# Optimization experiments

Measured on AMD Instinct MI355X. Metric: run time of the kernel, lower is better.

## Reference

```python
import jax, jax.numpy as jnp
import numpy as np

B, S, D, H, E, K = 4, 1024, 1024, 4096, 8, 2


def setup_inputs() -> dict:
    key = jax.random.key(0)
    ks = jax.random.split(key, 10)
    s = 0.02
    return {
        "x": jax.random.normal(ks[0], (B, S, D), jnp.float32),
        "noise": jax.random.normal(ks[1], (B, S, E), jnp.float32),
        "Wg": jax.random.normal(ks[2], (D, E), jnp.float32) * s,
        "bg": jnp.zeros((E,), jnp.float32),
        "Wn": jax.random.normal(ks[3], (D, E), jnp.float32) * s,
        "bn": jnp.zeros((E,), jnp.float32),
        "W1": jax.random.normal(ks[4], (E, D, H), jnp.float32) * s,
        "b1": jnp.zeros((E, H), jnp.float32),
        "W2": jax.random.normal(ks[5], (E, H, D), jnp.float32) * s,
        "b2": jnp.zeros((E, D), jnp.float32),
    }


def reference(x, noise, Wg, bg, Wn, bn, W1, b1, W2, b2):
    # --- noisy top-k gating ---
    logits = x @ Wg + bg                                   # [B,S,E]
    noisy = logits + noise * jax.nn.softplus(x @ Wn + bn)  # [B,S,E]
    topk_vals, topk_idx = jax.lax.top_k(noisy, K)          # [B,S,K]
    weights = jax.nn.softmax(topk_vals, axis=-1)           # [B,S,K]
    oh = jax.nn.one_hot(topk_idx, E, dtype=x.dtype)        # [B,S,K,E]
    mask = oh.sum(axis=-2)                                 # [B,S,E] 0/1 (topk idx distinct)
    w_full = (weights[..., None] * oh).sum(axis=-2)        # [B,S,E] combine weights

    # --- per-expert FFN (dense over experts, selected via w_full) ---
    h = jax.nn.gelu(jnp.einsum('bsd,edh->bseh', x, W1) + b1, approximate=False)
    eout = jnp.einsum('bseh,ehd->bsed', h, W2) + b2        # [B,S,E,D]
    combined = jnp.einsum('bse,bsed->bsd', w_full, eout)   # [B,S,D]

    # --- load balancing loss on clean gate probs ---
    gate_probs = jax.nn.softmax(logits, axis=-1)           # [B,S,E]
    expert_count = mask.sum(axis=(0, 1))                   # [E]
    total_tokens = mask.sum()
    expert_util = expert_count / total_tokens
    load_loss = jnp.sum(expert_util * gate_probs.mean(axis=(0, 1))) * E
    return combined, load_loss
```

## Files before the change

kernel.cpp:

```cpp
#include <hip/hip_runtime.h>
#include <hip/hip_bf16.h>

#define T_TOK 4096
#define D_DIM 1024
#define H_DIM 4096
#define E_EXP 8
#define K_TOP 2
#define TP (T_TOK * K_TOP)
#define BM 128
#define BN 128
#define BKS 32
#define MAX_TILES 72

typedef __attribute__((ext_vector_type(8))) short bf16x8;
typedef __attribute__((ext_vector_type(4))) float f32x4;
typedef __attribute__((ext_vector_type(8))) unsigned short u16x8;
typedef __attribute__((ext_vector_type(4))) unsigned short u16x4;

#define SWZ(row, chunk) ((chunk) ^ (((row) >> 1) & 3))

static __device__ __forceinline__ void gload16(const unsigned short* g, unsigned short* l) {
  __builtin_amdgcn_global_load_lds((const __attribute__((address_space(1))) void*)g,
                                   (__attribute__((address_space(3))) void*)l, 16, 0, 0);
}

static __device__ __forceinline__ unsigned short f2bf(float f) {
  unsigned int bits = __float_as_uint(f);
  unsigned int lsb = (bits >> 16) & 1u;
  bits += 0x7fffu + lsb;
  return (unsigned short)(bits >> 16);
}

static __device__ __forceinline__ float gelu_fast(float u) {
  float z = u * (0.79788456080286536f + 0.0356774081f * u * u);
  float t = __expf(-2.f * z);
  return u / (1.f + t);
}

#define NGATE (T_TOK / 4)
#define NTR1  ((H_DIM / 64) * (D_DIM / 64) * E_EXP)
#define NTR2  ((D_DIM / 64) * (H_DIM / 64) * E_EXP)

__global__ __launch_bounds__(256) void front_kernel(
    const float* __restrict__ W1, unsigned short* __restrict__ w1t,
    const float* __restrict__ W2, unsigned short* __restrict__ w2t,
    const float* __restrict__ x, const float* __restrict__ noise,
    const float* __restrict__ Wg, const float* __restrict__ bg,
    const float* __restrict__ Wn, const float* __restrict__ bn,
    int* __restrict__ tok_e, float* __restrict__ tok_w,
    float* __restrict__ gp_tok, int* __restrict__ counts,
    unsigned short* __restrict__ xb) {
  __shared__ float tile[64][65];
  int bid = blockIdx.x;
  const int tid = threadIdx.x;

  if (bid < NGATE) {
    const int lane = tid & 63, wid = tid >> 6;
    const int t = bid * 4 + wid;
    const float* xrow = x + (size_t)t * D_DIM;
    float ag[8] = {0, 0, 0, 0, 0, 0, 0, 0};
    float an[8] = {0, 0, 0, 0, 0, 0, 0, 0};
#pragma unroll 4
    for (int i = 0; i < 16; ++i) {
      int dd = i * 64 + lane;
      float xv = xrow[dd];
      xb[(size_t)t * D_DIM + dd] = f2bf(xv);
      const float4* g4 = (const float4*)(Wg + (size_t)dd * 8);
      const float4* n4 = (const float4*)(Wn + (size_t)dd * 8);
      float4 ga = g4[0], gb = g4[1], na = n4[0], nb = n4[1];
      ag[0] += xv * ga.x; ag[1] += xv * ga.y; ag[2] += xv * ga.z; ag[3] += xv * ga.w;
      ag[4] += xv * gb.x; ag[5] += xv * gb.y; ag[6] += xv * gb.z; ag[7] += xv * gb.w;
      an[0] += xv * na.x; an[1] += xv * na.y; an[2] += xv * na.z; an[3] += xv * na.w;
      an[4] += xv * nb.x; an[5] += xv * nb.y; an[6] += xv * nb.z; an[7] += xv * nb.w;
    }
#pragma unroll
    for (int e = 0; e < 8; ++e) {
      for (int off = 32; off > 0; off >>= 1) {
        ag[e] += __shfl_down(ag[e], off);
        an[e] += __shfl_down(an[e], off);
      }
    }
    if (lane == 0) {
      float logit[8], noisy[8];
#pragma unroll
      for (int e = 0; e < 8; ++e) {
        logit[e] = ag[e] + bg[e];
        float pre = an[e] + bn[e];
        float sp = fmaxf(pre, 0.f) + log1pf(expf(-fabsf(pre)));
        noisy[e] = logit[e] + noise[(size_t)t * 8 + e] * sp;
      }
      float mx = logit[0];
#pragma unroll
      for (int e = 1; e < 8; ++e) mx = fmaxf(mx, logit[e]);
      float s = 0.f, p[8];
#pragma unroll
      for (int e = 0; e < 8; ++e) { p[e] = expf(logit[e] - mx); s += p[e]; }
      float inv = 1.f / s;
#pragma unroll
      for (int e = 0; e < 8; ++e) gp_tok[(size_t)t * 8 + e] = p[e] * inv;
      int i0 = 0; float v0 = noisy[0];
#pragma unroll
      for (int e = 1; e < 8; ++e) if (noisy[e] > v0) { v0 = noisy[e]; i0 = e; }
      int i1 = -1; float v1 = 0.f;
#pragma unroll
      for (int e = 0; e < 8; ++e) {
        if (e == i0) continue;
        if (i1 < 0 || noisy[e] > v1) { v1 = noisy[e]; i1 = e; }
      }
      float e1 = expf(v1 - v0);
      float w0 = 1.f / (1.f + e1);
      float w1 = e1 * w0;
      tok_e[t * 2 + 0] = i0; tok_e[t * 2 + 1] = i1;
      tok_w[t * 2 + 0] = w0; tok_w[t * 2 + 1] = w1;
      atomicAdd(&counts[i0], 1);
      atomicAdd(&counts[i1], 1);
    }
    return;
  }
  bid -= NGATE;

  const float* src; unsigned short* dst; int R, C, bx, by, e;
  if (bid < NTR1) {
    R = D_DIM; C = H_DIM;
    bx = bid & 63; by = (bid >> 6) & 15; e = bid >> 10;
    src = W1; dst = w1t;
  } else {
    bid -= NTR1;
    R = H_DIM; C = D_DIM;
    bx = bid & 15; by = (bid >> 4) & 63; e = bid >> 10;
    src = W2; dst = w2t;
  }
  const int c0 = bx * 64, r0 = by * 64;
  const float* s = src + (size_t)e * R * C;
  unsigned short* d = dst + (size_t)e * R * C;

  const int rr = tid >> 4, c4 = tid & 15;
#pragma unroll
  for (int p = 0; p < 4; ++p) {
    int r = rr + p * 16;
    float4 v = *(const float4*)(&s[(size_t)(r0 + r) * C + c0 + c4 * 4]);
    tile[r][c4 * 4 + 0] = v.x;
    tile[r][c4 * 4 + 1] = v.y;
    tile[r][c4 * 4 + 2] = v.z;
    tile[r][c4 * 4 + 3] = v.w;
  }
  __syncthreads();
  const int cc = tid >> 3, r8 = tid & 7;
#pragma unroll
  for (int p = 0; p < 2; ++p) {
    int c = cc + p * 32;
    u16x8 o;
#pragma unroll
    for (int q = 0; q < 8; ++q) o[q] = f2bf(tile[r8 * 8 + q][c]);
    *(u16x8*)(&d[(size_t)(c0 + c) * R + r0 + r8 * 8]) = o;
  }
}

__global__ __launch_bounds__(256) void finalize_kernel(
    const int* __restrict__ counts, int4* __restrict__ tiles,
    int* __restrict__ ntiles,
    const int* __restrict__ tok_e, const float* __restrict__ tok_w,
    int* __restrict__ pair_token, float* __restrict__ pair_w,
    const float* __restrict__ gp_tok, float* __restrict__ out) {
  __shared__ int s_off[E_EXP];
  __shared__ int s_cur[E_EXP];
  __shared__ float red[256];
  const int tid = threadIdx.x;

  if (tid == 0) {
    int off = 0, nt = 0;
    for (int e = 0; e < E_EXP; ++e) {
      s_off[e] = off;
      int c = counts[e];
      for (int r = 0; r < c; r += BM) {
        tiles[nt] = make_int4(e, off + r, min(BM, c - r), 0);
        ++nt;
      }
      off += c;
    }
    *ntiles = nt;
  }
  if (tid < E_EXP) s_cur[tid] = 0;
  __syncthreads();

  for (int t = tid; t < T_TOK; t += 256) {
#pragma unroll
    for (int k = 0; k < 2; ++k) {
      int e = tok_e[t * 2 + k];
      int pos = atomicAdd(&s_cur[e], 1);
      int p = s_off[e] + pos;
      pair_token[p] = t;
      pair_w[p] = tok_w[t * 2 + k];
    }
  }

  float part[8] = {0, 0, 0, 0, 0, 0, 0, 0};
  for (int r = tid; r < T_TOK; r += 256) {
    const float* g = gp_tok + (size_t)r * 8;
#pragma unroll
    for (int e = 0; e < 8; ++e) part[e] += g[e];
  }
  float total[8];
#pragma unroll
  for (int e = 0; e < 8; ++e) {
    red[tid] = part[e];
    __syncthreads();
    for (int s = 128; s > 0; s >>= 1) {
      if (tid < s) red[tid] += red[tid + s];
      __syncthreads();
    }
    if (tid == 0) total[e] = red[0];
    __syncthreads();
  }
  if (tid == 0) {
    float ll = 0.f;
#pragma unroll
    for (int e = 0; e < 8; ++e)
      ll += ((float)counts[e] / (float)TP) * (total[e] / (float)T_TOK);
    out[(size_t)T_TOK * D_DIM] = ll * (float)E_EXP;
  }
}

__global__ __launch_bounds__(256) void ffn1_kernel(
    const unsigned short* __restrict__ xb,
    const unsigned short* __restrict__ w1t,
    const float* __restrict__ b1,
    const int* __restrict__ pair_token,
    const int4* __restrict__ tiles, const int* __restrict__ ntiles,
    unsigned short* __restrict__ hbuf) {
  const int NB = H_DIM / BN;
  const int nwg = MAX_TILES * NB;
  int bid = blockIdx.x;
  int wg = (bid & 7) * (nwg >> 3) + (bid >> 3);
  int tileId = wg / NB, nb = wg - tileId * NB;
  if (tileId >= *ntiles) return;
  int4 tl = tiles[tileId];
  const int e = tl.x, row0 = tl.y, rows = tl.z;
  const int n0 = nb * BN;

  __shared__ unsigned short sh[16384];
#define AS1(buf) (sh + (buf) * 4096)
#define BS1(buf) (sh + 8192 + (buf) * 4096)

  const int tid = threadIdx.x;
  const int wid = tid >> 6, lane = tid & 63;
  const int sr = tid >> 2;
  const int sc = tid & 3;
  const int scz = SWZ(sr, sc) * 8;

  int r0a = row0 + sr;       if (r0a > TP - 1) r0a = TP - 1;
  int r1a = row0 + sr + 64;  if (r1a > TP - 1) r1a = TP - 1;
  const unsigned short* a0 = xb + (size_t)pair_token[r0a] * D_DIM + scz;
  const unsigned short* a1 = xb + (size_t)pair_token[r1a] * D_DIM + scz;
  const unsigned short* bp0 = w1t + ((size_t)e * H_DIM + (n0 + sr)) * D_DIM + scz;
  const unsigned short* bp1 = w1t + ((size_t)e * H_DIM + (n0 + sr + 64)) * D_DIM + scz;

  const int wbase = wid * 512;
  const int wr = wid >> 1, wc = wid & 1;
  const int lrow = lane & 15, lkc = lane >> 4;

  f32x4 acc[4][4] = {};

  auto stage = [&](int buf, int k0) {
    gload16(a0 + k0, AS1(buf) + wbase);
    gload16(a1 + k0, AS1(buf) + wbase + 2048);
    gload16(bp0 + k0, BS1(buf) + wbase);
    gload16(bp1 + k0, BS1(buf) + wbase + 2048);
  };
  auto compute_step = [&](int buf) {
    bf16x8 af[4], bfr[4];
#pragma unroll
    for (int m = 0; m < 4; ++m) {
      int r = wr * 64 + m * 16 + lrow;
      af[m] = *(const bf16x8*)(AS1(buf) + r * BKS + SWZ(r, lkc) * 8);
    }
#pragma unroll
    for (int n = 0; n < 4; ++n) {
      int r = wc * 64 + n * 16 + lrow;
      bfr[n] = *(const bf16x8*)(BS1(buf) + r * BKS + SWZ(r, lkc) * 8);
    }
#pragma unroll
    for (int m = 0; m < 4; ++m)
#pragma unroll
      for (int n = 0; n < 4; ++n)
        acc[m][n] = __builtin_amdgcn_mfma_f32_16x16x32_bf16(af[m], bfr[n], acc[m][n], 0, 0, 0);
  };

  const int NK = D_DIM / BKS;
  stage(0, 0);
  stage(1, BKS);
  int cur = 0;
  for (int k = 0; k < NK - 1; ++k) {
    asm volatile("s_waitcnt vmcnt(4)" ::: "memory");
    __builtin_amdgcn_s_barrier();
    __builtin_amdgcn_sched_barrier(0);
    compute_step(cur);
    __builtin_amdgcn_sched_barrier(0);
    __builtin_amdgcn_s_barrier();
    if (k < NK - 2) stage(cur, (k + 2) * BKS);
    cur ^= 1;
  }
  asm volatile("s_waitcnt vmcnt(0)" ::: "memory");
  __builtin_amdgcn_s_barrier();
  __builtin_amdgcn_sched_barrier(0);
  compute_step(cur);

  __syncthreads();
#pragma unroll
  for (int n = 0; n < 4; ++n) {
    int clocal = wc * 64 + n * 16 + lrow;
    float bias = b1[(size_t)e * H_DIM + n0 + clocal];
    int chunk = clocal >> 3, within = clocal & 7;
#pragma unroll
    for (int m = 0; m < 4; ++m) {
#pragma unroll
      for (int j = 0; j < 4; ++j) {
        int rloc = wr * 64 + m * 16 + (lane >> 4) * 4 + j;
        float v = acc[m][n][j] + bias;
        sh[rloc * 128 + ((chunk ^ ((rloc >> 1) & 7)) * 8) + within] = f2bf(gelu_fast(v));
      }
    }
  }
  __syncthreads();
#pragma unroll
  for (int it = 0; it < 8; ++it) {
    int u = tid + 256 * it;
    int r = u >> 4, cg = u & 15;
    if (r < rows) {
      u16x8 v = *(const u16x8*)(&sh[r * 128 + ((cg ^ ((r >> 1) & 7)) * 8)]);
      *(u16x8*)(&hbuf[(size_t)(row0 + r) * H_DIM + n0 + cg * 8]) = v;
    }
  }
#undef AS1
#undef BS1
}

__global__ __launch_bounds__(256) void ffn2_kernel(
    const unsigned short* __restrict__ hbuf,
    const unsigned short* __restrict__ w2t,
    const float* __restrict__ b2,
    const int* __restrict__ pair_token, const float* __restrict__ pair_w,
    const int4* __restrict__ tiles, const int* __restrict__ ntiles,
    float* __restrict__ out) {
  const int NB = D_DIM / BN;
  const int nwg = MAX_TILES * NB;
  int bid = blockIdx.x;
  int wg = (bid & 7) * (nwg >> 3) + (bid >> 3);
  int tileId = wg / NB, nb = wg - tileId * NB;
  if (tileId >= *ntiles) return;
  int4 tl = tiles[tileId];
  const int e = tl.x, row0 = tl.y, rows = tl.z;
  const int n0 = nb * BN;

  __shared__ unsigned short As[2][BM * BKS];
  __shared__ unsigned short Bs[2][BN * BKS];
  __shared__ int stok[BM];
  __shared__ float spw[BM];

  const int tid = threadIdx.x;
  if (tid < BM) {
    int rr = row0 + tid; if (rr > TP - 1) rr = TP - 1;
    stok[tid] = pair_token[rr];
    spw[tid] = pair_w[rr];
  }

  const int wid = tid >> 6, lane = tid & 63;
  const int sr = tid >> 2;
  const int sc = tid & 3;
  const int scz = SWZ(sr, sc) * 8;

  int r0a = row0 + sr;       if (r0a > TP - 1) r0a = TP - 1;
  int r1a = row0 + sr + 64;  if (r1a > TP - 1) r1a = TP - 1;
  const unsigned short* a0 = hbuf + (size_t)r0a * H_DIM + scz;
  const unsigned short* a1 = hbuf + (size_t)r1a * H_DIM + scz;
  const unsigned short* bp0 = w2t + ((size_t)e * D_DIM + (n0 + sr)) * H_DIM + scz;
  const unsigned short* bp1 = w2t + ((size_t)e * D_DIM + (n0 + sr + 64)) * H_DIM + scz;

  const int wbase = wid * 512;
  const int wr = wid >> 1, wc = wid & 1;
  const int lrow = lane & 15, lkc = lane >> 4;

  f32x4 acc[4][4] = {};

  auto stage = [&](int buf, int k0) {
    gload16(a0 + k0, &As[buf][wbase]);
    gload16(a1 + k0, &As[buf][wbase + 2048]);
    gload16(bp0 + k0, &Bs[buf][wbase]);
    gload16(bp1 + k0, &Bs[buf][wbase + 2048]);
  };
  auto compute_step = [&](int buf) {
    bf16x8 af[4], bfr[4];
#pragma unroll
    for (int m = 0; m < 4; ++m) {
      int r = wr * 64 + m * 16 + lrow;
      af[m] = *(const bf16x8*)(&As[buf][r * BKS + SWZ(r, lkc) * 8]);
    }
#pragma unroll
    for (int n = 0; n < 4; ++n) {
      int r = wc * 64 + n * 16 + lrow;
      bfr[n] = *(const bf16x8*)(&Bs[buf][r * BKS + SWZ(r, lkc) * 8]);
    }
#pragma unroll
    for (int m = 0; m < 4; ++m)
#pragma unroll
      for (int n = 0; n < 4; ++n)
        acc[m][n] = __builtin_amdgcn_mfma_f32_16x16x32_bf16(af[m], bfr[n], acc[m][n], 0, 0, 0);
  };

  const int NK = H_DIM / BKS;
  stage(0, 0);
  stage(1, BKS);
  int cur = 0;
  for (int k = 0; k < NK - 1; ++k) {
    asm volatile("s_waitcnt vmcnt(4)" ::: "memory");
    __builtin_amdgcn_s_barrier();
    __builtin_amdgcn_sched_barrier(0);
    compute_step(cur);
    __builtin_amdgcn_sched_barrier(0);
    __builtin_amdgcn_s_barrier();
    if (k < NK - 2) stage(cur, (k + 2) * BKS);
    cur ^= 1;
  }
  asm volatile("s_waitcnt vmcnt(0)" ::: "memory");
  __builtin_amdgcn_s_barrier();
  __builtin_amdgcn_sched_barrier(0);
  compute_step(cur);

  const int colbase = n0 + wc * 64;
#pragma unroll
  for (int n = 0; n < 4; ++n) {
    int colg = colbase + n * 16 + lrow;
    float bias = b2[(size_t)e * D_DIM + colg];
#pragma unroll
    for (int m = 0; m < 4; ++m) {
      int rbase = wr * 64 + m * 16 + (lane >> 4) * 4;
#pragma unroll
      for (int j = 0; j < 4; ++j) {
        int rloc = rbase + j;
        if (rloc < rows) {
          float v = acc[m][n][j] + bias;
          unsafeAtomicAdd(&out[(size_t)stok[rloc] * D_DIM + colg], spw[rloc] * v);
        }
      }
    }
  }
}

extern "C" void kernel_launch(void* const* d_in, const int* in_sizes, int n_in,
                              void* d_out, int out_size, void* d_ws, size_t ws_size,
                              hipStream_t stream) {
  (void)in_sizes; (void)n_in; (void)ws_size;
  const float* x     = (const float*)d_in[0];
  const float* noise = (const float*)d_in[1];
  const float* Wg    = (const float*)d_in[2];
  const float* bg    = (const float*)d_in[3];
  const float* Wn    = (const float*)d_in[4];
  const float* bn    = (const float*)d_in[5];
  const float* W1    = (const float*)d_in[6];
  const float* b1    = (const float*)d_in[7];
  const float* W2    = (const float*)d_in[8];
  const float* b2    = (const float*)d_in[9];
  float* out = (float*)d_out;

  char* ws = (char*)d_ws;
  size_t o = 0;
  auto take = [&](size_t b) { size_t r = o; o += (b + 255) & ~(size_t)255; return r; };
  int*   counts     = (int*)(ws + take(16 * 4));
  int*   ntiles     = (int*)(ws + take(4));
  int4*  tiles      = (int4*)(ws + take(MAX_TILES * 16));
  int*   tok_e      = (int*)(ws + take((size_t)TP * 4));
  float* tok_w      = (float*)(ws + take((size_t)TP * 4));
  float* gp_tok     = (float*)(ws + take((size_t)T_TOK * 8 * 4));
  int*   pair_token = (int*)(ws + take((size_t)TP * 4));
  float* pair_w     = (float*)(ws + take((size_t)TP * 4));
  unsigned short* xb  = (unsigned short*)(ws + take((size_t)T_TOK * D_DIM * 2));
  unsigned short* w1t = (unsigned short*)(ws + take((size_t)E_EXP * H_DIM * D_DIM * 2));
  unsigned short* w2t = (unsigned short*)(ws + take((size_t)E_EXP * H_DIM * D_DIM * 2));
  unsigned short* hbuf = (unsigned short*)(ws + take((size_t)TP * H_DIM * 2));

  hipMemsetAsync(d_out, 0, (size_t)out_size * sizeof(float), stream);
  hipMemsetAsync(counts, 0, 16 * 4, stream);

  front_kernel<<<NGATE + NTR1 + NTR2, 256, 0, stream>>>(
      W1, w1t, W2, w2t, x, noise, Wg, bg, Wn, bn,
      tok_e, tok_w, gp_tok, counts, xb);
  finalize_kernel<<<1, 256, 0, stream>>>(counts, tiles, ntiles, tok_e, tok_w,
                                         pair_token, pair_w, gp_tok, out);
  ffn1_kernel<<<dim3(MAX_TILES * (H_DIM / BN)), 256, 0, stream>>>(
      xb, w1t, b1, pair_token, tiles, ntiles, hbuf);
  ffn2_kernel<<<dim3(MAX_TILES * (D_DIM / BN)), 256, 0, stream>>>(
      hbuf, w2t, b2, pair_token, pair_w, tiles, ntiles, out);
}
```

Measured before the change: 437.2 us.

## Move W2 transpose into ffn1 launch and widen transpose tiles to 128

The W2 fp32-to-bf16 transpose now runs as extra leading blocks of the ffn1 kernel instead of in the front kernel, so it can overlap with the FFN1 GEMM. Both weight transposes also switch to 128x128 tiles that convert to bf16 before writing a padded LDS tile, which halves LDS traffic per element and cuts block count. The risk is that the transpose blocks delay FFN1 tiles, and ffn1's shared memory grows slightly, which may lower occupancy.

```diff
diff --git a/kernel.cpp b/kernel.cpp
--- a/kernel.cpp
+++ b/kernel.cpp
@@ -37,20 +37,45 @@
   return u / (1.f + t);
 }
 
+static __device__ __forceinline__ void transpose128_body(
+    const float* __restrict__ s, unsigned short* __restrict__ d, int R, int C,
+    int c0, int r0, unsigned short* tile_b, int tid) {
+#pragma unroll
+  for (int p = 0; p < 16; ++p) {
+    int u = tid + 256 * p;
+    int row = u >> 5, c4 = u & 31;
+    float4 v = *(const float4*)(&s[(size_t)(r0 + row) * C + c0 + c4 * 4]);
+    int base = row * 130 + c4 * 4;
+    tile_b[base + 0] = f2bf(v.x);
+    tile_b[base + 1] = f2bf(v.y);
+    tile_b[base + 2] = f2bf(v.z);
+    tile_b[base + 3] = f2bf(v.w);
+  }
+  __syncthreads();
+#pragma unroll
+  for (int p = 0; p < 8; ++p) {
+    int u = tid + 256 * p;
+    int c = u >> 4, rq = u & 15;
+    u16x8 o;
+#pragma unroll
+    for (int q = 0; q < 8; ++q) o[q] = tile_b[(rq * 8 + q) * 130 + c];
+    *(u16x8*)(&d[(size_t)(c0 + c) * R + r0 + rq * 8]) = o;
+  }
+}
+
 #define NGATE (T_TOK / 4)
-#define NTR1  ((H_DIM / 64) * (D_DIM / 64) * E_EXP)
-#define NTR2  ((D_DIM / 64) * (H_DIM / 64) * E_EXP)
+#define NTRW1 ((H_DIM / 128) * (D_DIM / 128) * E_EXP)
+#define NTRW2 ((D_DIM / 128) * (H_DIM / 128) * E_EXP)
 
 __global__ __launch_bounds__(256) void front_kernel(
     const float* __restrict__ W1, unsigned short* __restrict__ w1t,
-    const float* __restrict__ W2, unsigned short* __restrict__ w2t,
     const float* __restrict__ x, const float* __restrict__ noise,
     const float* __restrict__ Wg, const float* __restrict__ bg,
     const float* __restrict__ Wn, const float* __restrict__ bn,
     int* __restrict__ tok_e, float* __restrict__ tok_w,
     float* __restrict__ gp_tok, int* __restrict__ counts,
     unsigned short* __restrict__ xb) {
-  __shared__ float tile[64][65];
+  __shared__ unsigned short tile_b[128 * 130];
   int bid = blockIdx.x;
   const int tid = threadIdx.x;
 
@@ -118,42 +143,10 @@
     return;
   }
   bid -= NGATE;
-
-  const float* src; unsigned short* dst; int R, C, bx, by, e;
-  if (bid < NTR1) {
-    R = D_DIM; C = H_DIM;
-    bx = bid & 63; by = (bid >> 6) & 15; e = bid >> 10;
-    src = W1; dst = w1t;
-  } else {
-    bid -= NTR1;
-    R = H_DIM; C = D_DIM;
-    bx = bid & 15; by = (bid >> 4) & 63; e = bid >> 10;
-    src = W2; dst = w2t;
-  }
-  const int c0 = bx * 64, r0 = by * 64;
-  const float* s = src + (size_t)e * R * C;
-  unsigned short* d = dst + (size_t)e * R * C;
-
-  const int rr = tid >> 4, c4 = tid & 15;
-#pragma unroll
-  for (int p = 0; p < 4; ++p) {
-    int r = rr + p * 16;
-    float4 v = *(const float4*)(&s[(size_t)(r0 + r) * C + c0 + c4 * 4]);
-    tile[r][c4 * 4 + 0] = v.x;
-    tile[r][c4 * 4 + 1] = v.y;
-    tile[r][c4 * 4 + 2] = v.z;
-    tile[r][c4 * 4 + 3] = v.w;
-  }
-  __syncthreads();
-  const int cc = tid >> 3, r8 = tid & 7;
-#pragma unroll
-  for (int p = 0; p < 2; ++p) {
-    int c = cc + p * 32;
-    u16x8 o;
-#pragma unroll
-    for (int q = 0; q < 8; ++q) o[q] = f2bf(tile[r8 * 8 + q][c]);
-    *(u16x8*)(&d[(size_t)(c0 + c) * R + r0 + r8 * 8]) = o;
-  }
+  const int bx = bid & 31, by = (bid >> 5) & 7, e = bid >> 8;
+  transpose128_body(W1 + (size_t)e * D_DIM * H_DIM,
+                    w1t + (size_t)e * D_DIM * H_DIM,
+                    D_DIM, H_DIM, bx * 128, by * 128, tile_b, tid);
 }
 
 __global__ __launch_bounds__(256) void finalize_kernel(
@@ -227,10 +220,23 @@
     const float* __restrict__ b1,
     const int* __restrict__ pair_token,
     const int4* __restrict__ tiles, const int* __restrict__ ntiles,
-    unsigned short* __restrict__ hbuf) {
+    unsigned short* __restrict__ hbuf,
+    const float* __restrict__ W2, unsigned short* __restrict__ w2t) {
+  __shared__ unsigned short sh[16640];
+  const int tid = threadIdx.x;
+  int bid = blockIdx.x;
+
+  if (bid < NTRW2) {
+    const int bx = bid & 7, by = (bid >> 3) & 31, e = bid >> 8;
+    transpose128_body(W2 + (size_t)e * D_DIM * H_DIM,
+                      w2t + (size_t)e * D_DIM * H_DIM,
+                      H_DIM, D_DIM, bx * 128, by * 128, sh, tid);
+    return;
+  }
+  bid -= NTRW2;
+
   const int NB = H_DIM / BN;
   const int nwg = MAX_TILES * NB;
-  int bid = blockIdx.x;
   int wg = (bid & 7) * (nwg >> 3) + (bid >> 3);
   int tileId = wg / NB, nb = wg - tileId * NB;
   if (tileId >= *ntiles) return;
@@ -238,11 +244,9 @@
   const int e = tl.x, row0 = tl.y, rows = tl.z;
   const int n0 = nb * BN;
 
-  __shared__ unsigned short sh[16384];
 #define AS1(buf) (sh + (buf) * 4096)
 #define BS1(buf) (sh + 8192 + (buf) * 4096)
 
-  const int tid = threadIdx.x;
   const int wid = tid >> 6, lane = tid & 63;
   const int sr = tid >> 2;
   const int sc = tid & 3;
@@ -481,13 +485,12 @@
   hipMemsetAsync(d_out, 0, (size_t)out_size * sizeof(float), stream);
   hipMemsetAsync(counts, 0, 16 * 4, stream);
 
-  front_kernel<<<NGATE + NTR1 + NTR2, 256, 0, stream>>>(
-      W1, w1t, W2, w2t, x, noise, Wg, bg, Wn, bn,
-      tok_e, tok_w, gp_tok, counts, xb);
+  front_kernel<<<NGATE + NTRW1, 256, 0, stream>>>(
+      W1, w1t, x, noise, Wg, bg, Wn, bn, tok_e, tok_w, gp_tok, counts, xb);
   finalize_kernel<<<1, 256, 0, stream>>>(counts, tiles, ntiles, tok_e, tok_w,
                                          pair_token, pair_w, gp_tok, out);
-  ffn1_kernel<<<dim3(MAX_TILES * (H_DIM / BN)), 256, 0, stream>>>(
-      xb, w1t, b1, pair_token, tiles, ntiles, hbuf);
+  ffn1_kernel<<<NTRW2 + MAX_TILES * (H_DIM / BN), 256, 0, stream>>>(
+      xb, w1t, b1, pair_token, tiles, ntiles, hbuf, W2, w2t);
   ffn2_kernel<<<dim3(MAX_TILES * (D_DIM / BN)), 256, 0, stream>>>(
       hbuf, w2t, b2, pair_token, pair_w, tiles, ntiles, out);
 }
```

New measurement: 441.2 us. Within noise of the previous version (+0.9%).
